# Kernel tuning notes

Hardware: AMD Instinct MI355X
Metric: run time of the kernel (lower is better)

The kernel has to match this reference:

```python
import jax, jax.numpy as jnp
import numpy as np

N, E = 50000, 800000
NODE_DIM, EDGE_DIM, HEADS = 64, 16, 4
C = NODE_DIM // HEADS  # per-head channels
NEG_SLOPE = 0.2
BN_EPS = 1e-5


def setup_inputs() -> dict:
    key = jax.random.key(0)
    ks = jax.random.split(key, 12)
    glorot = lambda k, shape: jax.random.normal(k, shape, jnp.float32) * np.sqrt(2.0 / (shape[0] + shape[-1]))
    return {
        "x": jax.random.normal(ks[0], (N, NODE_DIM), jnp.float32),
        "edge_index": jax.random.randint(ks[1], (2, E), 0, N, jnp.int32),
        "edge_attr": jax.random.normal(ks[2], (E, EDGE_DIM), jnp.float32),
        "W_l": glorot(ks[3], (NODE_DIM, HEADS * C)),
        "b_l": jnp.zeros((HEADS * C,), jnp.float32),
        "W_r": glorot(ks[4], (NODE_DIM, HEADS * C)),
        "b_r": jnp.zeros((HEADS * C,), jnp.float32),
        "W_e": glorot(ks[5], (EDGE_DIM, HEADS * C)),
        "att": glorot(ks[6], (HEADS, C)),
        "bias": jnp.zeros((HEADS * C,), jnp.float32),
        "gamma": jnp.ones((NODE_DIM,), jnp.float32),
        "beta": jnp.zeros((NODE_DIM,), jnp.float32),
    }


def reference(x, edge_index, edge_attr, W_l, b_l, W_r, b_r, W_e, att, bias, gamma, beta):
    src, dst = edge_index[0], edge_index[1]
    n = x.shape[0]
    # GATv2: node transforms for source (l) and target (r) roles
    xl = (x @ W_l + b_l).reshape(n, HEADS, C)
    xr = (x @ W_r + b_r).reshape(n, HEADS, C)
    e = (edge_attr @ W_e).reshape(-1, HEADS, C)
    # per-edge attention logits: leaky_relu(x_j + x_i + e) . att  -> [E, H]
    g = jax.nn.leaky_relu(xl[src] + xr[dst] + e, NEG_SLOPE)
    logits = jnp.einsum('ehc,hc->eh', g, att)
    # segment softmax grouped by destination node
    amax = jax.ops.segment_max(logits, dst, num_segments=n)
    ex = jnp.exp(logits - amax[dst])
    denom = jax.ops.segment_sum(ex, dst, num_segments=n)
    alpha = ex / (denom[dst] + 1e-16)  # [E, H]
    # weighted message aggregation (scatter-add over dst), concat heads
    msg = xl[src] * alpha[..., None]  # [E, H, C]
    out = jax.ops.segment_sum(msg, dst, num_segments=n).reshape(n, HEADS * C) + bias
    # BatchNorm (training-mode batch statistics over nodes)
    mean = out.mean(axis=0)
    var = out.var(axis=0)
    out = (out - mean) * jax.lax.rsqrt(var + BN_EPS) * gamma + beta
    # residual + exact GELU
    return jax.nn.gelu(out + x, approximate=False)
```

## Files before the change

### kernel.cpp

```cpp
#include <hip/hip_runtime.h>
#include <hip/hip_fp16.h>
#include <math.h>

#define NODE_DIM 64
#define EDGE_DIM 16
#define CAP 64
#define NEG_SLOPE 0.2f
#define BN_EPS 1e-5f

typedef unsigned short ushort_t;
typedef unsigned int uint_t;

__device__ __forceinline__ float wave_max64(float v) {
#pragma unroll
    for (int o = 32; o; o >>= 1) v = fmaxf(v, __shfl_xor(v, o, 64));
    return v;
}
__device__ __forceinline__ float wave_sum64(float v) {
#pragma unroll
    for (int o = 32; o; o >>= 1) v += __shfl_xor(v, o, 64);
    return v;
}
__device__ __forceinline__ ushort_t f2bf(float f) {
    unsigned int b = __float_as_uint(f);
    b += 0x7FFFu + ((b >> 16) & 1u);
    return (ushort_t)(b >> 16);
}
__device__ __forceinline__ float bf2f(ushort_t u) {
    return __uint_as_float(((unsigned int)u) << 16);
}
__device__ __forceinline__ uint_t packh2(float a, float b) {
    __half2 h;
    h.x = __float2half_rn(a);
    h.y = __float2half_rn(b);
    return *reinterpret_cast<uint_t*>(&h);
}
__device__ __forceinline__ float2 unpackh2(uint_t u) {
    __half2 h = *reinterpret_cast<__half2*>(&u);
    return make_float2(__half2float(h.x), __half2float(h.y));
}

__global__ __launch_bounds__(256) void k_transform(
    const float* __restrict__ x, const float* __restrict__ Wl,
    const float* __restrict__ bl, const float* __restrict__ Wr,
    const float* __restrict__ br, ushort_t* __restrict__ xlbf,
    ushort_t* __restrict__ xrbf, int n)
{
    __shared__ float sWl[NODE_DIM * NODE_DIM];
    __shared__ float sWr[NODE_DIM * NODE_DIM];
    for (int i = threadIdx.x; i < NODE_DIM * NODE_DIM; i += 256) {
        sWl[i] = Wl[i];
        sWr[i] = Wr[i];
    }
    __syncthreads();
    int lane = threadIdx.x & 63;
    int wid = threadIdx.x >> 6;
    for (int row = blockIdx.x * 4 + wid; row < n; row += gridDim.x * 4) {
        float xown = x[(size_t)row * NODE_DIM + lane];
        float al = bl[lane], ar = br[lane];
#pragma unroll
        for (int k = 0; k < NODE_DIM; k++) {
            float xv = __shfl(xown, k, 64);
            al = fmaf(xv, sWl[k * 64 + lane], al);
            ar = fmaf(xv, sWr[k * 64 + lane], ar);
        }
        xlbf[(size_t)row * NODE_DIM + lane] = f2bf(al);
        xrbf[(size_t)row * NODE_DIM + lane] = f2bf(ar);
    }
}

__global__ __launch_bounds__(256) void k_edge(
    const int* __restrict__ ei, const float* __restrict__ eattr,
    const float* __restrict__ We, const float* __restrict__ att,
    int* __restrict__ cursors,
    const ushort_t* __restrict__ xlbf, const ushort_t* __restrict__ xrbf,
    int* __restrict__ slots, uint4* __restrict__ payload, int E)
{
    __shared__ float sea[4][64 * EDGE_DIM];
    __shared__ float slg[4][64 * 4];

    int lane = threadIdx.x & 63;
    int wid = threadIdx.x >> 6;
    int wbase = (blockIdx.x * 4 + wid) * 64;
    if (wbase >= E) return;
    wbase = __builtin_amdgcn_readfirstlane(wbase);
    int cnt = E - wbase; if (cnt > 64) cnt = 64;

    {
        const float4* esrc = (const float4*)(eattr + (size_t)wbase * EDGE_DIM);
        float4* sdst = (float4*)sea[wid];
        int lim = cnt * 4;
#pragma unroll
        for (int r = 0; r < 4; r++) {
            int idx = r * 64 + lane;
            if (idx < lim) sdst[idx] = esrc[idx];
        }
    }

    float we_c[EDGE_DIM];
#pragma unroll
    for (int k = 0; k < EDGE_DIM; k++) we_c[k] = We[k * NODE_DIM + lane];
    float att_p = att[lane];
    float att_n = att_p * NEG_SLOPE;

    int src_l = 0;
    if (lane < cnt) {
        src_l = ei[wbase + lane];
        int dst_l = ei[E + wbase + lane];
        int pos_l = atomicAdd(&cursors[dst_l], 1);
        if (pos_l < CAP) slots[(size_t)dst_l * CAP + pos_l] = wbase + lane;
    }
    int dst_l_bc = (lane < cnt) ? ei[E + wbase + lane] : 0;

    float* seaW = sea[wid];
    float* slgW = slg[wid];

    ushort_t pxl[16], pxr[16];
    auto LOADT = [&](int t, int k) {
        int s = __builtin_amdgcn_readlane(src_l, t);
        int d = __builtin_amdgcn_readlane(dst_l_bc, t);
        pxl[k] = xlbf[(size_t)s * NODE_DIM + lane];
        pxr[k] = xrbf[(size_t)d * NODE_DIM + lane];
    };
    auto COMP = [&](int t, int k) {
        const float4* e4 = (const float4*)(seaW + t * EDGE_DIM);
        float4 a0 = e4[0], a1 = e4[1], a2 = e4[2], a3 = e4[3];
        float p0 = 0.f, p1 = 0.f;
        p0 = fmaf(a0.x, we_c[0], p0);  p1 = fmaf(a0.y, we_c[1], p1);
        p0 = fmaf(a0.z, we_c[2], p0);  p1 = fmaf(a0.w, we_c[3], p1);
        p0 = fmaf(a1.x, we_c[4], p0);  p1 = fmaf(a1.y, we_c[5], p1);
        p0 = fmaf(a1.z, we_c[6], p0);  p1 = fmaf(a1.w, we_c[7], p1);
        p0 = fmaf(a2.x, we_c[8], p0);  p1 = fmaf(a2.y, we_c[9], p1);
        p0 = fmaf(a2.z, we_c[10], p0); p1 = fmaf(a2.w, we_c[11], p1);
        p0 = fmaf(a3.x, we_c[12], p0); p1 = fmaf(a3.y, we_c[13], p1);
        p0 = fmaf(a3.z, we_c[14], p0); p1 = fmaf(a3.w, we_c[15], p1);
        float sv = bf2f(pxl[k]) + bf2f(pxr[k]) + (p0 + p1);
        float g = sv * (sv > 0.f ? att_p : att_n);
        g += __shfl_xor(g, 1, 64);
        g += __shfl_xor(g, 2, 64);
        g += __shfl_xor(g, 4, 64);
        g += __shfl_xor(g, 8, 64);
        if ((lane & 15) == 0) slgW[t * 4 + (lane >> 4)] = g;
    };

    if (cnt == 64) {
#pragma unroll
        for (int k = 0; k < 16; k++) LOADT(k, k);
#pragma unroll
        for (int tb = 0; tb < 48; tb += 16) {
#pragma unroll
            for (int k = 0; k < 16; k++) {
                COMP(tb + k, k);
                LOADT(tb + k + 16, k);
            }
        }
#pragma unroll
        for (int k = 0; k < 16; k++) COMP(48 + k, k);
    } else {
        ushort_t qxl[8], qxr[8];
        auto LOADQ = [&](int t, int k) {
            int s = __builtin_amdgcn_readlane(src_l, t);
            int d = __builtin_amdgcn_readlane(dst_l_bc, t);
            qxl[k] = xlbf[(size_t)s * NODE_DIM + lane];
            qxr[k] = xrbf[(size_t)d * NODE_DIM + lane];
        };
        auto COMPQ = [&](int t, int k) {
            pxl[0] = qxl[k]; pxr[0] = qxr[k];
            COMP(t, 0);
        };
#pragma unroll
        for (int k = 0; k < 8; k++) if (k < cnt) LOADQ(k, k);
        for (int tb = 0; tb < cnt; tb += 8) {
#pragma unroll
            for (int k = 0; k < 8; k++) {
                int t = tb + k;
                if (t < cnt) {
                    COMPQ(t, k);
                    int tn = t + 8;
                    if (tn < cnt) LOADQ(tn, k);
                }
            }
        }
    }

    if (lane < cnt) {
        float4 lg4 = ((const float4*)slgW)[lane];
        payload[wbase + lane] =
            make_uint4((uint_t)src_l, packh2(lg4.x, lg4.y),
                       packh2(lg4.z, lg4.w), 0u);
    }
}

__global__ __launch_bounds__(256) void k_fused(
    const int* __restrict__ slots, const uint4* __restrict__ payload,
    const int* __restrict__ cursors, const ushort_t* __restrict__ xlbf,
    const float* __restrict__ bias, float* __restrict__ out, int n)
{
    __shared__ float salpha[4][CAP * 4];

    int wid = threadIdx.x >> 6;
    int lane = threadIdx.x & 63;
    int i = blockIdx.x * 4 + wid;
    if (i >= n) return;

    int deg = cursors[i];
    if (deg > CAP) deg = CAP;
    bool act = (lane < deg);

    int eid = act ? slots[(size_t)i * CAP + lane] : 0;
    uint4 pl = act ? payload[eid] : make_uint4(0u, 0u, 0u, 0u);
    int se_x = (int)pl.x;
    float2 g01 = unpackh2(pl.y);
    float2 g23 = unpackh2(pl.z);

    float l0 = act ? g01.x : -1e30f;
    float l1 = act ? g01.y : -1e30f;
    float l2 = act ? g23.x : -1e30f;
    float l3 = act ? g23.y : -1e30f;
    float m0 = wave_max64(l0), m1 = wave_max64(l1);
    float m2 = wave_max64(l2), m3 = wave_max64(l3);
    float e0 = act ? __expf(l0 - m0) : 0.f;
    float e1 = act ? __expf(l1 - m1) : 0.f;
    float e2 = act ? __expf(l2 - m2) : 0.f;
    float e3 = act ? __expf(l3 - m3) : 0.f;
    float s0 = wave_sum64(e0), s1 = wave_sum64(e1);
    float s2 = wave_sum64(e2), s3 = wave_sum64(e3);
    float* salW = salpha[wid];
    ((float4*)salW)[lane] = make_float4(
        e0 / (s0 + 1e-16f), e1 / (s1 + 1e-16f),
        e2 / (s2 + 1e-16f), e3 / (s3 + 1e-16f));

    int h = lane >> 4;
    float acc0 = 0.f, acc1 = 0.f;
    ushort_t cp[32];
    auto CLOAD = [&](int t, int k) {
        int s = __builtin_amdgcn_readlane(se_x, t);
        cp[k] = xlbf[(size_t)s * NODE_DIM + lane];
    };
    int degR = (deg + 7) & ~7;

#define PROLOG(B)                                                        \
    if ((B) < degR) {                                                    \
        _Pragma("unroll")                                                \
        for (int j = 0; j < 8; j++) CLOAD((B) + j, (B) + j);             \
    }
    PROLOG(0) PROLOG(8) PROLOG(16) PROLOG(24)
#undef PROLOG

#define SUB(B)                                                           \
    if (tb + (B) < degR) {                                               \
        _Pragma("unroll")                                                \
        for (int j = 0; j < 8; j++) {                                    \
            int t = tb + (B) + j;                                        \
            float a = salW[t * 4 + h];                                   \
            if (((B) + j) & 1) acc1 = fmaf(a, bf2f(cp[(B) + j]), acc1);  \
            else               acc0 = fmaf(a, bf2f(cp[(B) + j]), acc0);  \
            int tn = t + 32;                                             \
            if (tn < degR) CLOAD(tn, (B) + j);                           \
        }                                                                \
    }
    for (int tb = 0; tb < degR; tb += 32) {
        SUB(0) SUB(8) SUB(16) SUB(24)
    }
#undef SUB

    out[(size_t)i * NODE_DIM + lane] = acc0 + acc1 + bias[lane];
}

__global__ __launch_bounds__(256) void k_bnstat(
    const float* __restrict__ out, float* __restrict__ stats, int n)
{
    __shared__ float sbuf[256];
    int col = threadIdx.x & 63;
    int rgrp = threadIdx.x >> 6;
    float s = 0.f, q = 0.f;
    for (int row = blockIdx.x * 4 + rgrp; row < n; row += gridDim.x * 4) {
        float v = out[(size_t)row * 64 + col];
        s += v;
        q = fmaf(v, v, q);
    }
    sbuf[threadIdx.x] = s;
    __syncthreads();
    if (threadIdx.x < 64) {
        s = sbuf[threadIdx.x] + sbuf[threadIdx.x + 64] +
            sbuf[threadIdx.x + 128] + sbuf[threadIdx.x + 192];
        atomicAdd(&stats[col], s);
    }
    __syncthreads();
    sbuf[threadIdx.x] = q;
    __syncthreads();
    if (threadIdx.x < 64) {
        q = sbuf[threadIdx.x] + sbuf[threadIdx.x + 64] +
            sbuf[threadIdx.x + 128] + sbuf[threadIdx.x + 192];
        atomicAdd(&stats[64 + col], q);
    }
}

__global__ __launch_bounds__(256) void k_final(
    float* __restrict__ out, const float* __restrict__ x,
    const float* __restrict__ stats, const float* __restrict__ gamma,
    const float* __restrict__ beta, int total, float invn)
{
    int i = blockIdx.x * 256 + threadIdx.x;
    if (i >= total) return;
    int c = i & 63;
    float mean = stats[c] * invn;
    float var = stats[64 + c] * invn - mean * mean;
    float z = (out[i] - mean) * rsqrtf(var + BN_EPS) * gamma[c] + beta[c] + x[i];
    out[i] = z * 0.5f * (1.f + erff(z * 0.70710678118654752f));
}

extern "C" void kernel_launch(void* const* d_in, const int* in_sizes, int n_in,
                              void* d_out, int out_size, void* d_ws, size_t ws_size,
                              hipStream_t stream)
{
    const float* x     = (const float*)d_in[0];
    const int*   ei    = (const int*)d_in[1];
    const float* eattr = (const float*)d_in[2];
    const float* Wl    = (const float*)d_in[3];
    const float* bl    = (const float*)d_in[4];
    const float* Wr    = (const float*)d_in[5];
    const float* br    = (const float*)d_in[6];
    const float* We    = (const float*)d_in[7];
    const float* att   = (const float*)d_in[8];
    const float* bias  = (const float*)d_in[9];
    const float* gamma = (const float*)d_in[10];
    const float* beta  = (const float*)d_in[11];
    int n = in_sizes[0] / NODE_DIM;
    int E = in_sizes[1] / 2;

    char* ws = (char*)d_ws;
    ushort_t* xlbf    = (ushort_t*)ws; ws += (size_t)n * NODE_DIM * 2;
    ushort_t* xrbf    = (ushort_t*)ws; ws += (size_t)n * NODE_DIM * 2;
    uint4*    payload = (uint4*)ws;    ws += (size_t)E * 16;
    int*      slots   = (int*)ws;      ws += (size_t)n * CAP * 4;
    int*      cursors = (int*)ws;      ws += (size_t)n * 4;
    float*    stats   = (float*)ws;    ws += 128 * 4;

    hipMemsetAsync(cursors, 0, (size_t)(n + 128) * 4, stream);

    k_transform<<<512, 256, 0, stream>>>(x, Wl, bl, Wr, br, xlbf, xrbf, n);
    k_edge<<<(E + 255) / 256, 256, 0, stream>>>(
        ei, eattr, We, att, cursors, xlbf, xrbf, slots, payload, E);
    k_fused<<<(n + 3) / 4, 256, 0, stream>>>(
        slots, payload, cursors, xlbf, bias, (float*)d_out, n);
    k_bnstat<<<256, 256, 0, stream>>>((const float*)d_out, stats, n);
    k_final<<<(n * NODE_DIM + 255) / 256, 256, 0, stream>>>(
        (float*)d_out, x, stats, gamma, beta, n * NODE_DIM, 1.0f / n);
}
```

Baseline: 202.8 us.

## Read edge attributes directly from global memory and shrink gather prefetch depth

Removes the per-wave LDS staging of edge attributes. Each edge's 16 attribute floats are now read from global memory with wave-uniform addresses, which the compiler can turn into scalar loads. The software-pipelined gather prefetch depth drops from 16 to 8 edges, and the main loop is no longer unrolled, to cut code size and register pressure. The risk is extra per-edge load latency exposed on the edge-attribute reads and less latency hiding for the random xl/xr gathers.

```diff
diff --git a/kernel.cpp b/kernel.cpp
--- a/kernel.cpp
+++ b/kernel.cpp
@@ -76,7 +76,6 @@
     const ushort_t* __restrict__ xlbf, const ushort_t* __restrict__ xrbf,
     int* __restrict__ slots, uint4* __restrict__ payload, int E)
 {
-    __shared__ float sea[4][64 * EDGE_DIM];
     __shared__ float slg[4][64 * 4];
 
     int lane = threadIdx.x & 63;
@@ -86,17 +85,6 @@
     wbase = __builtin_amdgcn_readfirstlane(wbase);
     int cnt = E - wbase; if (cnt > 64) cnt = 64;
 
-    {
-        const float4* esrc = (const float4*)(eattr + (size_t)wbase * EDGE_DIM);
-        float4* sdst = (float4*)sea[wid];
-        int lim = cnt * 4;
-#pragma unroll
-        for (int r = 0; r < 4; r++) {
-            int idx = r * 64 + lane;
-            if (idx < lim) sdst[idx] = esrc[idx];
-        }
-    }
-
     float we_c[EDGE_DIM];
 #pragma unroll
     for (int k = 0; k < EDGE_DIM; k++) we_c[k] = We[k * NODE_DIM + lane];
@@ -112,10 +100,9 @@
     }
     int dst_l_bc = (lane < cnt) ? ei[E + wbase + lane] : 0;
 
-    float* seaW = sea[wid];
     float* slgW = slg[wid];
 
-    ushort_t pxl[16], pxr[16];
+    ushort_t pxl[8], pxr[8];
     auto LOADT = [&](int t, int k) {
         int s = __builtin_amdgcn_readlane(src_l, t);
         int d = __builtin_amdgcn_readlane(dst_l_bc, t);
@@ -123,17 +110,13 @@
         pxr[k] = xrbf[(size_t)d * NODE_DIM + lane];
     };
     auto COMP = [&](int t, int k) {
-        const float4* e4 = (const float4*)(seaW + t * EDGE_DIM);
-        float4 a0 = e4[0], a1 = e4[1], a2 = e4[2], a3 = e4[3];
+        const float* ear = eattr + (size_t)(wbase + t) * EDGE_DIM;
         float p0 = 0.f, p1 = 0.f;
-        p0 = fmaf(a0.x, we_c[0], p0);  p1 = fmaf(a0.y, we_c[1], p1);
-        p0 = fmaf(a0.z, we_c[2], p0);  p1 = fmaf(a0.w, we_c[3], p1);
-        p0 = fmaf(a1.x, we_c[4], p0);  p1 = fmaf(a1.y, we_c[5], p1);
-        p0 = fmaf(a1.z, we_c[6], p0);  p1 = fmaf(a1.w, we_c[7], p1);
-        p0 = fmaf(a2.x, we_c[8], p0);  p1 = fmaf(a2.y, we_c[9], p1);
-        p0 = fmaf(a2.z, we_c[10], p0); p1 = fmaf(a2.w, we_c[11], p1);
-        p0 = fmaf(a3.x, we_c[12], p0); p1 = fmaf(a3.y, we_c[13], p1);
-        p0 = fmaf(a3.z, we_c[14], p0); p1 = fmaf(a3.w, we_c[15], p1);
+#pragma unroll
+        for (int kk = 0; kk < EDGE_DIM; kk += 2) {
+            p0 = fmaf(ear[kk],     we_c[kk],     p0);
+            p1 = fmaf(ear[kk + 1], we_c[kk + 1], p1);
+        }
         float sv = bf2f(pxl[k]) + bf2f(pxr[k]) + (p0 + p1);
         float g = sv * (sv > 0.f ? att_p : att_n);
         g += __shfl_xor(g, 1, 64);
@@ -145,39 +128,28 @@
 
     if (cnt == 64) {
 #pragma unroll
-        for (int k = 0; k < 16; k++) LOADT(k, k);
-#pragma unroll
-        for (int tb = 0; tb < 48; tb += 16) {
-#pragma unroll
-            for (int k = 0; k < 16; k++) {
+        for (int k = 0; k < 8; k++) LOADT(k, k);
+#pragma unroll 1
+        for (int tb = 0; tb < 56; tb += 8) {
+#pragma unroll
+            for (int k = 0; k < 8; k++) {
                 COMP(tb + k, k);
-                LOADT(tb + k + 16, k);
+                LOADT(tb + k + 8, k);
             }
         }
 #pragma unroll
-        for (int k = 0; k < 16; k++) COMP(48 + k, k);
+        for (int k = 0; k < 8; k++) COMP(56 + k, k);
     } else {
-        ushort_t qxl[8], qxr[8];
-        auto LOADQ = [&](int t, int k) {
-            int s = __builtin_amdgcn_readlane(src_l, t);
-            int d = __builtin_amdgcn_readlane(dst_l_bc, t);
-            qxl[k] = xlbf[(size_t)s * NODE_DIM + lane];
-            qxr[k] = xrbf[(size_t)d * NODE_DIM + lane];
-        };
-        auto COMPQ = [&](int t, int k) {
-            pxl[0] = qxl[k]; pxr[0] = qxr[k];
-            COMP(t, 0);
-        };
-#pragma unroll
-        for (int k = 0; k < 8; k++) if (k < cnt) LOADQ(k, k);
+#pragma unroll
+        for (int k = 0; k < 8; k++) if (k < cnt) LOADT(k, k);
         for (int tb = 0; tb < cnt; tb += 8) {
 #pragma unroll
             for (int k = 0; k < 8; k++) {
                 int t = tb + k;
                 if (t < cnt) {
-                    COMPQ(t, k);
+                    COMP(t, k);
                     int tn = t + 8;
-                    if (tn < cnt) LOADQ(tn, k);
+                    if (tn < cnt) LOADT(tn, k);
                 }
             }
         }
```

Result: slower. 209.4 us (+3.3%).
